# Performance work log

Measured on AMD Instinct MI355X. Metric: run time of the kernel, lower is better.

Reference implementation:

```python
import jax, jax.numpy as jnp
import numpy as np

NB_OBJ = 16
BATCH = 64
F_IN = 32768
HID = 64
N_AGENTS = 4
N_ACT = 13
NEG_SLOPE = 0.01  # torch LeakyReLU default


def _build_edges():
    # fully connected minus diagonal, per graph; GCNConv adds self-loops
    adj = np.ones((NB_OBJ, NB_OBJ)) - np.eye(NB_OBJ)
    r, c = np.nonzero(adj)
    loop = np.arange(NB_OBJ)
    src = np.concatenate([r, loop])
    dst = np.concatenate([c, loop])
    offs = (np.arange(BATCH) * NB_OBJ)[:, None]
    src_all = (src[None, :] + offs).reshape(-1)
    dst_all = (dst[None, :] + offs).reshape(-1)
    return jnp.asarray(src_all, jnp.int32), jnp.asarray(dst_all, jnp.int32)


def setup_inputs() -> dict:
    key = jax.random.key(0)
    ks = jax.random.split(key, 9)
    s = 1.0 / np.sqrt(F_IN)
    sh = 1.0 / np.sqrt(HID)
    return {
        "unary_tensor": jax.random.normal(ks[0], (BATCH, NB_OBJ, F_IN), jnp.float32),
        "binary_tensor": jax.random.uniform(ks[1], (BATCH, NB_OBJ, NB_OBJ, 2), jnp.float32),
        "actions": jax.random.normal(ks[2], (N_AGENTS, BATCH, N_ACT), jnp.float32),
        "gcn_w": jax.random.uniform(ks[3], (F_IN, HID), jnp.float32, -s, s),
        "gcn_b": jax.random.uniform(ks[4], (HID,), jnp.float32, -s, s),
        "head_w1": jax.random.uniform(ks[5], (N_AGENTS, HID, HID), jnp.float32, -sh, sh),
        "head_b1": jax.random.uniform(ks[6], (N_AGENTS, HID), jnp.float32, -sh, sh),
        "head_w2": jax.random.uniform(ks[7], (N_AGENTS, HID, N_ACT), jnp.float32, -sh, sh),
        "head_b2": jax.random.uniform(ks[8], (N_AGENTS, N_ACT), jnp.float32, -sh, sh),
    }


def reference(unary_tensor, binary_tensor, actions, gcn_w, gcn_b,
              head_w1, head_b1, head_w2, head_b2):
    src, dst = _build_edges()
    x = unary_tensor.reshape(BATCH * NB_OBJ, F_IN)  # flatten(0,1)
    lin = x @ gcn_w  # [1024, HID]
    # GCN symmetric norm: every node has degree 16 (15 neighbors + self loop)
    norm = 1.0 / NB_OBJ
    msg = lin[src] * norm
    agg = jax.ops.segment_sum(msg, dst, num_segments=BATCH * NB_OBJ)
    h = agg + gcn_b  # [1024, HID]
    # split into graphs and max-pool over nodes
    pooled = jnp.max(h.reshape(BATCH, NB_OBJ, HID), axis=1)  # [64, HID]
    # per-agent critic heads
    z = jnp.einsum('bh,ahk->abk', pooled, head_w1) + head_b1[:, None, :]
    z = jnp.where(z >= 0, z, NEG_SLOPE * z)  # LeakyReLU
    all_q = jnp.einsum('abh,ahk->abk', z, head_w2) + head_b2[:, None, :]  # [A,64,13]
    int_acs = jnp.argmax(actions, axis=2)  # [A, 64]
    q = jnp.take_along_axis(all_q, int_acs[:, :, None], axis=2)  # [A, 64, 1]
    return q
```

## Files before the change

### kernel.cpp

```cpp
#include <hip/hip_runtime.h>

#define F_IN    32768
#define HID     64
#define NB_OBJ  16
#define BATCH   64
#define N_AGENTS 4
#define N_ACT   13
#define NEG_SLOPE 0.01f

#define FC      64
#define NCHUNK  (F_IN / FC)

typedef float f32x4 __attribute__((ext_vector_type(4)));

__device__ float g_part[BATCH * NCHUNK * HID];

__global__ __launch_bounds__(512, 4)
void k_fused(const float* __restrict__ u, const float* __restrict__ w) {
    __shared__ float xbar[BATCH][FC + 4];
    const int t    = threadIdx.x;
    const int blk  = blockIdx.x;
    const int f0   = blk * FC;
    const int lane = t & 63;
    const int wv   = t >> 6;

    float wreg[FC];
    {
        const float* wp = w + (size_t)f0 * HID + lane;
        #pragma unroll
        for (int f = 0; f < FC; ++f) wreg[f] = wp[f * HID];
    }

    {
        const int b = t >> 3;
        const int j = t & 7;
        const float* up = u + (size_t)b * (NB_OBJ * F_IN) + f0 + j * 4;
        f32x4 a0 = (f32x4)(0.f);
        f32x4 a1 = (f32x4)(0.f);
        #pragma unroll
        for (int o = 0; o < NB_OBJ; ++o) {
            const float* ro = up + (size_t)o * F_IN;
            a0 += *reinterpret_cast<const f32x4*>(ro);
            a1 += *reinterpret_cast<const f32x4*>(ro + 32);
        }
        const float inv = 1.0f / (float)NB_OBJ;
        a0 *= inv;
        a1 *= inv;
        *reinterpret_cast<f32x4*>(&xbar[b][j * 4])      = a0;
        *reinterpret_cast<f32x4*>(&xbar[b][32 + j * 4]) = a1;
    }
    __syncthreads();

    {
        #pragma unroll
        for (int bb = 0; bb < 8; ++bb) {
            const int b = wv * 8 + bb;
            float acc = 0.f;
            #pragma unroll
            for (int fq = 0; fq < FC / 4; ++fq) {
                f32x4 xb = *reinterpret_cast<const f32x4*>(&xbar[b][fq * 4]);
                acc += xb.x * wreg[fq * 4 + 0];
                acc += xb.y * wreg[fq * 4 + 1];
                acc += xb.z * wreg[fq * 4 + 2];
                acc += xb.w * wreg[fq * 4 + 3];
            }
            g_part[((size_t)b * NCHUNK + blk) * HID + lane] = acc;
        }
    }
}

__global__ __launch_bounds__(1024)
void k_tail(const float* __restrict__ gcn_b,
            const float* __restrict__ w1, const float* __restrict__ b1,
            const float* __restrict__ w2, const float* __restrict__ b2,
            const float* __restrict__ actions, float* __restrict__ out) {
    const int b = blockIdx.x;
    const int t = threadIdx.x;
    __shared__ float red[16][HID];
    __shared__ float pooled[HID];
    __shared__ float zbuf[N_AGENTS][HID];
    __shared__ float qbuf[N_AGENTS][N_ACT];

    {
        const int h  = t & 63;
        const int kg = t >> 6;
        const float* p = g_part + ((size_t)b * NCHUNK + kg * 32) * HID + h;
        float acc = 0.f;
        #pragma unroll
        for (int i = 0; i < 32; ++i)
            acc += p[(size_t)i * HID];
        red[kg][h] = acc;
    }
    __syncthreads();
    if (t < HID) {
        float acc = gcn_b[t];
        #pragma unroll
        for (int kg = 0; kg < 16; ++kg) acc += red[kg][t];
        pooled[t] = acc;
    }
    __syncthreads();

    if (t < N_AGENTS * HID) {
        const int a = t >> 6, k = t & 63;
        const float* w1p = w1 + a * (HID * HID) + k;
        float acc = b1[a * HID + k];
        #pragma unroll
        for (int hh = 0; hh < HID; ++hh) acc += pooled[hh] * w1p[hh * HID];
        zbuf[a][k] = (acc >= 0.f) ? acc : NEG_SLOPE * acc;
    }
    __syncthreads();

    if (t < N_AGENTS * N_ACT) {
        const int a = t / N_ACT, c = t % N_ACT;
        const float* w2p = w2 + a * (HID * N_ACT) + c;
        float acc = b2[a * N_ACT + c];
        #pragma unroll
        for (int hh = 0; hh < HID; ++hh) acc += zbuf[a][hh] * w2p[hh * N_ACT];
        qbuf[a][c] = acc;
    }
    __syncthreads();

    if (t < N_AGENTS) {
        const float* ap = actions + ((size_t)t * BATCH + b) * N_ACT;
        int best = 0; float bv = ap[0];
        for (int c = 1; c < N_ACT; ++c) {
            float v = ap[c];
            if (v > bv) { bv = v; best = c; }
        }
        out[t * BATCH + b] = qbuf[t][best];
    }
}

extern "C" void kernel_launch(void* const* d_in, const int* in_sizes, int n_in,
                              void* d_out, int out_size, void* d_ws, size_t ws_size,
                              hipStream_t stream) {
    const float* u   = (const float*)d_in[0];
    const float* act = (const float*)d_in[2];
    const float* gw  = (const float*)d_in[3];
    const float* gb  = (const float*)d_in[4];
    const float* w1  = (const float*)d_in[5];
    const float* b1  = (const float*)d_in[6];
    const float* w2  = (const float*)d_in[7];
    const float* b2  = (const float*)d_in[8];
    float* out = (float*)d_out;

    hipLaunchKernelGGL(k_fused, dim3(NCHUNK), dim3(512), 0, stream, u, gw);
    hipLaunchKernelGGL(k_tail,  dim3(BATCH),  dim3(1024), 0, stream,
                       gb, w1, b1, w2, b2, act, out);
}
```

Measured before the change: 36.16 us.

## Double feature chunk per block, use 1024 threads, and add nontemporal loads

Feature chunk per block grows from 64 to 128, so there are half as many blocks, each with 1024 threads, and half as many partial sums for the tail kernel to reduce. Weights are now loaded in two 64-row sub-chunks inside the compute loop, which keeps register use per thread at about the same level. The big unary tensor is read with nontemporal loads to avoid polluting the cache. The risks are lower occupancy with 1024-thread blocks at 4 blocks per CU (likely not achievable) and only 256 blocks to fill the GPU.

```diff
diff --git a/kernel.cpp b/kernel.cpp
--- a/kernel.cpp
+++ b/kernel.cpp
@@ -8,14 +8,14 @@
 #define N_ACT   13
 #define NEG_SLOPE 0.01f
 
-#define FC      64
+#define FC      128
 #define NCHUNK  (F_IN / FC)
 
 typedef float f32x4 __attribute__((ext_vector_type(4)));
 
 __device__ float g_part[BATCH * NCHUNK * HID];
 
-__global__ __launch_bounds__(512, 4)
+__global__ __launch_bounds__(1024, 4)
 void k_fused(const float* __restrict__ u, const float* __restrict__ w) {
     __shared__ float xbar[BATCH][FC + 4];
     const int t    = threadIdx.x;
@@ -24,48 +24,54 @@
     const int lane = t & 63;
     const int wv   = t >> 6;
 
-    float wreg[FC];
     {
-        const float* wp = w + (size_t)f0 * HID + lane;
-        #pragma unroll
-        for (int f = 0; f < FC; ++f) wreg[f] = wp[f * HID];
-    }
-
-    {
-        const int b = t >> 3;
-        const int j = t & 7;
+        const int b = t >> 4;
+        const int j = t & 15;
         const float* up = u + (size_t)b * (NB_OBJ * F_IN) + f0 + j * 4;
         f32x4 a0 = (f32x4)(0.f);
         f32x4 a1 = (f32x4)(0.f);
         #pragma unroll
         for (int o = 0; o < NB_OBJ; ++o) {
             const float* ro = up + (size_t)o * F_IN;
-            a0 += *reinterpret_cast<const f32x4*>(ro);
-            a1 += *reinterpret_cast<const f32x4*>(ro + 32);
+            a0 += __builtin_nontemporal_load(reinterpret_cast<const f32x4*>(ro));
+            a1 += __builtin_nontemporal_load(reinterpret_cast<const f32x4*>(ro + 64));
         }
         const float inv = 1.0f / (float)NB_OBJ;
         a0 *= inv;
         a1 *= inv;
         *reinterpret_cast<f32x4*>(&xbar[b][j * 4])      = a0;
-        *reinterpret_cast<f32x4*>(&xbar[b][32 + j * 4]) = a1;
+        *reinterpret_cast<f32x4*>(&xbar[b][64 + j * 4]) = a1;
     }
     __syncthreads();
 
-    {
+    float acc[4] = {0.f, 0.f, 0.f, 0.f};
+    #pragma unroll
+    for (int sc = 0; sc < 2; ++sc) {
+        float wreg[64];
+        {
+            const float* wp = w + (size_t)(f0 + sc * 64) * HID + lane;
+            #pragma unroll
+            for (int f = 0; f < 64; ++f) wreg[f] = wp[f * HID];
+        }
         #pragma unroll
-        for (int bb = 0; bb < 8; ++bb) {
-            const int b = wv * 8 + bb;
-            float acc = 0.f;
+        for (int bb = 0; bb < 4; ++bb) {
+            const int b = wv * 4 + bb;
+            float a = 0.f;
             #pragma unroll
-            for (int fq = 0; fq < FC / 4; ++fq) {
-                f32x4 xb = *reinterpret_cast<const f32x4*>(&xbar[b][fq * 4]);
-                acc += xb.x * wreg[fq * 4 + 0];
-                acc += xb.y * wreg[fq * 4 + 1];
-                acc += xb.z * wreg[fq * 4 + 2];
-                acc += xb.w * wreg[fq * 4 + 3];
+            for (int fq = 0; fq < 16; ++fq) {
+                f32x4 xb = *reinterpret_cast<const f32x4*>(&xbar[b][sc * 64 + fq * 4]);
+                a += xb.x * wreg[fq * 4 + 0];
+                a += xb.y * wreg[fq * 4 + 1];
+                a += xb.z * wreg[fq * 4 + 2];
+                a += xb.w * wreg[fq * 4 + 3];
             }
-            g_part[((size_t)b * NCHUNK + blk) * HID + lane] = acc;
+            acc[bb] += a;
         }
+    }
+    #pragma unroll
+    for (int bb = 0; bb < 4; ++bb) {
+        const int b = wv * 4 + bb;
+        g_part[((size_t)b * NCHUNK + blk) * HID + lane] = acc[bb];
     }
 }
 
@@ -84,10 +90,10 @@
     {
         const int h  = t & 63;
         const int kg = t >> 6;
-        const float* p = g_part + ((size_t)b * NCHUNK + kg * 32) * HID + h;
+        const float* p = g_part + ((size_t)b * NCHUNK + kg * 16) * HID + h;
         float acc = 0.f;
         #pragma unroll
-        for (int i = 0; i < 32; ++i)
+        for (int i = 0; i < 16; ++i)
             acc += p[(size_t)i * HID];
         red[kg][h] = acc;
     }
@@ -144,7 +150,7 @@
     const float* b2  = (const float*)d_in[8];
     float* out = (float*)d_out;
 
-    hipLaunchKernelGGL(k_fused, dim3(NCHUNK), dim3(512), 0, stream, u, gw);
+    hipLaunchKernelGGL(k_fused, dim3(NCHUNK), dim3(1024), 0, stream, u, gw);
     hipLaunchKernelGGL(k_tail,  dim3(BATCH),  dim3(1024), 0, stream,
                        gb, w1, b1, w2, b2, act, out);
 }
```

After: 37.32 us. +3.2%, slower.

## Remap per-chunk GEMV to lane-per-batch with wave-uniform weight loads and swizzled LDS

Applied to the files above, without the earlier changes.

Each block's small matmul is remapped so that each lane owns one batch row and each wave owns 8 hidden outputs. The weights are then read as wave-uniform (scalar-broadcast) loads instead of 64 per-thread registers, and xbar reads become per-lane vector loads. The shared-memory layout gets an XOR swizzle instead of padding to avoid bank conflicts, and the results are transposed back through LDS with an extra sync before the coalesced store. This is meant to cut register pressure and LDS traffic in the compute phase. The cost is more synchronisation and uniform global loads of weights from cache.

```diff
diff --git a/kernel.cpp b/kernel.cpp
--- a/kernel.cpp
+++ b/kernel.cpp
@@ -17,23 +17,17 @@
 
 __global__ __launch_bounds__(512, 4)
 void k_fused(const float* __restrict__ u, const float* __restrict__ w) {
-    __shared__ float xbar[BATCH][FC + 4];
+    __shared__ float xbar[BATCH * FC];
     const int t    = threadIdx.x;
     const int blk  = blockIdx.x;
     const int f0   = blk * FC;
     const int lane = t & 63;
     const int wv   = t >> 6;
 
-    float wreg[FC];
     {
-        const float* wp = w + (size_t)f0 * HID + lane;
-        #pragma unroll
-        for (int f = 0; f < FC; ++f) wreg[f] = wp[f * HID];
-    }
-
-    {
-        const int b = t >> 3;
-        const int j = t & 7;
+        const int b  = t >> 3;
+        const int j  = t & 7;
+        const int bq = b & 7;
         const float* up = u + (size_t)b * (NB_OBJ * F_IN) + f0 + j * 4;
         f32x4 a0 = (f32x4)(0.f);
         f32x4 a1 = (f32x4)(0.f);
@@ -46,25 +40,51 @@
         const float inv = 1.0f / (float)NB_OBJ;
         a0 *= inv;
         a1 *= inv;
-        *reinterpret_cast<f32x4*>(&xbar[b][j * 4])      = a0;
-        *reinterpret_cast<f32x4*>(&xbar[b][32 + j * 4]) = a1;
+        *reinterpret_cast<f32x4*>(&xbar[b * 64 + ((j ^ bq) << 2)])      = a0;
+        *reinterpret_cast<f32x4*>(&xbar[b * 64 + ((j ^ bq) << 2) + 32]) = a1;
+    }
+    __syncthreads();
+
+    const int h0 = __builtin_amdgcn_readfirstlane(wv) * 8;
+    const int bq = lane & 7;
+    f32x4 accA = (f32x4)(0.f), accB = (f32x4)(0.f);
+    #pragma unroll
+    for (int g = 0; g < 8; ++g) {
+        f32x4 x0 = *reinterpret_cast<const f32x4*>(
+            &xbar[lane * 64 + (((2 * g) ^ bq) << 2)]);
+        f32x4 x1 = *reinterpret_cast<const f32x4*>(
+            &xbar[lane * 64 + (((2 * g + 1) ^ bq) << 2)]);
+        #pragma unroll
+        for (int e = 0; e < 4; ++e) {
+            const float* wp = w + (size_t)(f0 + 8 * g + e) * HID + h0;
+            #pragma unroll
+            for (int k = 0; k < 4; ++k) accA[k] += x0[e] * wp[k];
+            #pragma unroll
+            for (int k = 0; k < 4; ++k) accB[k] += x0[e] * wp[4 + k];
+        }
+        #pragma unroll
+        for (int e = 0; e < 4; ++e) {
+            const float* wp = w + (size_t)(f0 + 8 * g + 4 + e) * HID + h0;
+            #pragma unroll
+            for (int k = 0; k < 4; ++k) accA[k] += x1[e] * wp[k];
+            #pragma unroll
+            for (int k = 0; k < 4; ++k) accB[k] += x1[e] * wp[4 + k];
+        }
     }
     __syncthreads();
 
     {
+        const int q0 = h0 >> 2;
+        *reinterpret_cast<f32x4*>(&xbar[lane * 64 + ((q0 ^ bq) << 2)])       = accA;
+        *reinterpret_cast<f32x4*>(&xbar[lane * 64 + (((q0 + 1) ^ bq) << 2)]) = accB;
+    }
+    __syncthreads();
+    {
         #pragma unroll
         for (int bb = 0; bb < 8; ++bb) {
             const int b = wv * 8 + bb;
-            float acc = 0.f;
-            #pragma unroll
-            for (int fq = 0; fq < FC / 4; ++fq) {
-                f32x4 xb = *reinterpret_cast<const f32x4*>(&xbar[b][fq * 4]);
-                acc += xb.x * wreg[fq * 4 + 0];
-                acc += xb.y * wreg[fq * 4 + 1];
-                acc += xb.z * wreg[fq * 4 + 2];
-                acc += xb.w * wreg[fq * 4 + 3];
-            }
-            g_part[((size_t)b * NCHUNK + blk) * HID + lane] = acc;
+            float v = xbar[b * 64 + ((((lane >> 2) ^ bb)) << 2) + (lane & 3)];
+            g_part[((size_t)b * NCHUNK + blk) * HID + lane] = v;
         }
     }
 }
@@ -144,7 +164,7 @@
     const float* b2  = (const float*)d_in[8];
     float* out = (float*)d_out;
 
-    hipLaunchKernelGGL(k_fused, dim3(NCHUNK), dim3(512), 0, stream, u, gw);
+    hipLaunchKernelGGL(k_fused, dim3(NCHUNK), dim3(512),  0, stream, u, gw);
     hipLaunchKernelGGL(k_tail,  dim3(BATCH),  dim3(1024), 0, stream,
                        gb, w1, b1, w2, b2, act, out);
 }
```

Result: slower. 38.35 us (+6.1%).
